# Optimization experiments

Hardware: AMD Instinct MI355X
Metric: run time of the kernel (lower is better)

Reference implementation:

```python
import math
import jax, jax.numpy as jnp
import numpy as np

B, N, D, H, L = 8, 1024, 512, 8, 6
HD = D // H
FREQ = 256
K_LORENTZ = 1.0


def lorentz_projx(x, k=K_LORENTZ):
    # geoopt Lorentz.projx: x0 = sqrt(k + ||x_space||^2)
    space = x[..., 1:]
    x0 = jnp.sqrt(k + jnp.sum(space * space, axis=-1, keepdims=True))
    return jnp.concatenate([x0, space], axis=-1)


def layernorm(x, eps=1e-6):
    m = jnp.mean(x, axis=-1, keepdims=True)
    v = jnp.mean((x - m) ** 2, axis=-1, keepdims=True)
    return (x - m) / jnp.sqrt(v + eps)


def make_pe(n, d):
    pos = np.arange(n, dtype=np.float32)[:, None]
    div = np.exp(np.arange(0, d, 2, dtype=np.float32) * (-math.log(10000.0) / d))
    pe = np.zeros((n, d), dtype=np.float32)
    pe[:, 0::2] = np.sin(pos * div)
    pe[:, 1::2] = np.cos(pos * div)
    return jnp.asarray(pe)


def setup_inputs() -> dict:
    key = jax.random.key(0)
    ks = jax.random.split(key, 20)
    s = 0.02
    inp = {
        "t": jax.random.uniform(ks[0], (B,), jnp.float32) * 1000.0,
        "x": jax.random.normal(ks[1], (B, N, D), jnp.float32),
        "mask": jnp.ones((B, N), jnp.float32),
        "pe": make_pe(N, D),
        # timestep embedder MLP (weights stored [in,out])
        "tw1": jax.random.normal(ks[2], (FREQ, D), jnp.float32) * s,
        "tb1": jnp.zeros((D,), jnp.float32),
        "tw2": jax.random.normal(ks[3], (D, D), jnp.float32) * s,
        "tb2": jnp.zeros((D,), jnp.float32),
        # per-layer params stacked over L
        "Wq": jax.random.normal(ks[4], (L, D, D), jnp.float32) * s,
        "bq": jnp.zeros((L, D), jnp.float32),
        "Wk": jax.random.normal(ks[5], (L, D, D), jnp.float32) * s,
        "bk": jnp.zeros((L, D), jnp.float32),
        "Wv": jax.random.normal(ks[6], (L, D, D), jnp.float32) * s,
        "bv": jnp.zeros((L, D), jnp.float32),
        "W1": jax.random.normal(ks[7], (L, D, 4 * D), jnp.float32) * s,
        "b1": jnp.zeros((L, 4 * D), jnp.float32),
        "W2": jax.random.normal(ks[8], (L, 4 * D, D), jnp.float32) * s,
        "b2": jnp.zeros((L, D), jnp.float32),
        "Wada": jax.random.normal(ks[9], (L, D, 6 * D), jnp.float32) * s,
        "bada": jnp.zeros((L, 6 * D), jnp.float32),
    }
    return inp


def timestep_embedding(t, dim=FREQ, max_period=10000.0):
    half = dim // 2
    freqs = jnp.exp(-math.log(max_period) * jnp.arange(half, dtype=jnp.float32) / half)
    args = t[:, None] * freqs[None]
    return jnp.concatenate([jnp.cos(args), jnp.sin(args)], axis=-1)  # [B, dim]


def attention(h, mask, Wq, bq, Wk, bk, Wv, bv):
    # h: [B,N,D], mask: [B,N]
    q = (h @ Wq + bq).reshape(B, N, H, HD).transpose(0, 2, 1, 3)
    k = (h @ Wk + bk).reshape(B, N, H, HD).transpose(0, 2, 1, 3)
    v = (h @ Wv + bv).reshape(B, N, H, HD).transpose(0, 2, 1, 3)
    scores = jnp.einsum("bhqd,bhkd->bhqk", q, k) / math.sqrt(HD)
    # faithful quirk: valid positions get +1 added, invalid get -10000
    mm = jnp.einsum("bi,bj->bij", mask, mask)[:, None]  # [B,1,N,N]
    mm = jnp.where(mm == 0, -10000.0, mm)
    scores = scores + mm
    probs = jax.nn.softmax(scores, axis=-1)
    ctx = jnp.einsum("bhqk,bhkd->bhqd", probs, v)
    return ctx.transpose(0, 2, 1, 3).reshape(B, N, D)


def reference(t, x, mask, pe, tw1, tb1, tw2, tb2, Wq, bq, Wk, bk, Wv, bv,
              W1, b1, W2, b2, Wada, bada):
    # z = x + PositionalEncoding(x) = 2*x + pe
    z = x + (x + pe[None])
    # timestep embedder
    c = timestep_embedding(t) @ tw1 + tb1
    c = jax.nn.silu(c) @ tw2 + tb2  # [B, D]
    for i in range(L):
        ada = jax.nn.silu(c) @ Wada[i] + bada[i]  # [B, 6D]
        sh_msa, sc_msa, g_msa, sh_mlp, sc_mlp, g_mlp = jnp.split(ada, 6, axis=-1)
        h = layernorm(z) * (1.0 + sc_msa[:, None]) + sh_msa[:, None]
        z = z + g_msa[:, None] * attention(h, mask, Wq[i], bq[i], Wk[i], bk[i], Wv[i], bv[i])
        z = lorentz_projx(z)
        h = layernorm(z) * (1.0 + sc_mlp[:, None]) + sh_mlp[:, None]
        m = jax.nn.gelu(h @ W1[i] + b1[i], approximate=True) @ W2[i] + b2[i]
        z = z + g_mlp[:, None] * m
        z = lorentz_projx(z)
    z = lorentz_projx(z)
    return jnp.where(mask[:, :, None] != 0, z, 0.0)
```

## Files before the change

kernel.cpp:

```cpp
#include <hip/hip_runtime.h>
#include <hip/hip_bf16.h>
#include <math.h>

#define NTOK 1024
#define DMODEL 512
#define NHEAD 8
#define HDIM 64
#define BATCH 8
#define NLAYER 6
#define ROWS (BATCH*NTOK)
#define QKVSTR 1536
#define LOG2E 1.44269504f

typedef __attribute__((ext_vector_type(8))) short bf16x8;
typedef __attribute__((ext_vector_type(4))) float f32x4;
typedef unsigned short ushort_t;


__device__ __forceinline__ float silu_f(float x) { return x / (1.f + expf(-x)); }

__device__ __forceinline__ float gelu_tanh_f(float x) {
    float x3 = x * x * x;
    float y2 = 1.5957691216057308f * (x + 0.044715f * x3);
    float e = __builtin_amdgcn_exp2f(-y2 * LOG2E);
    return x / (1.f + e);
}

__device__ __forceinline__ unsigned short f2bf(float x) {
    __hip_bfloat16 b = __float2bfloat16(x);
    return *reinterpret_cast<unsigned short*>(&b);
}

__device__ __forceinline__ float bf2f(unsigned short u) {
    union { float f; unsigned v; } c;
    c.v = (unsigned)u << 16;
    return c.f;
}

__device__ __forceinline__ float wave_sum(float v) {
    #pragma unroll
    for (int o = 1; o < 64; o <<= 1) v += __shfl_xor(v, o);
    return v;
}


__global__ __launch_bounds__(256) void init_z_kernel(const float* __restrict__ x,
                                                     const float* __restrict__ pe,
                                                     float* __restrict__ z) {
    int i = blockIdx.x * 256 + threadIdx.x;
    const int C4 = DMODEL / 4;
    int row = i / C4;
    int col4 = i - row * C4;
    int n = row & (NTOK - 1);
    float4 xv = ((const float4*)x)[i];
    float4 pv = ((const float4*)pe)[n * C4 + col4];
    float4 o;
    o.x = 2.f * xv.x + pv.x;
    o.y = 2.f * xv.y + pv.y;
    o.z = 2.f * xv.z + pv.z;
    o.w = 2.f * xv.w + pv.w;
    ((float4*)z)[i] = o;
}

__global__ void temb_kernel(const float* __restrict__ t, float* __restrict__ temb) {
    int b = blockIdx.x;
    int j = threadIdx.x;
    float f = expf(-9.210340371976184f * (float)j / 128.f);
    float a = t[b] * f;
    temb[b * 256 + j] = cosf(a);
    temb[b * 256 + 128 + j] = sinf(a);
}

__global__ void zero512(float* __restrict__ p) {
    p[blockIdx.x * 256 + threadIdx.x] = 0.f;
}

__global__ __launch_bounds__(256) void skinny_part(const float* __restrict__ A,
                                                   const float* __restrict__ W,
                                                   float* __restrict__ part,
                                                   int K, int N, int NL) {
    __shared__ float Als[8][128];
    const int l = blockIdx.z;
    const int n = blockIdx.x * 256 + threadIdx.x;
    const int kc = blockIdx.y;
    const int kbase = kc * 128;
    for (int i = threadIdx.x; i < 8 * 128; i += 256) {
        int b = i >> 7, k = i & 127;
        Als[b][k] = A[b * K + kbase + k];
    }
    __syncthreads();
    float acc[8] = {};
    const float* wp = W + (size_t)l * K * N + (size_t)kbase * N + n;
    for (int k = 0; k < 128; k += 4) {
        float w0 = wp[0];
        float w1 = wp[N];
        float w2 = wp[2 * N];
        float w3 = wp[3 * N];
        wp += 4 * (size_t)N;
        #pragma unroll
        for (int b = 0; b < 8; b++)
            acc[b] += Als[b][k] * w0 + Als[b][k + 1] * w1 + Als[b][k + 2] * w2 + Als[b][k + 3] * w3;
    }
    #pragma unroll
    for (int b = 0; b < 8; b++)
        part[((size_t)kc * 8 + b) * NL + (size_t)l * N + n] = acc[b];
}

template<int ACT>
__global__ __launch_bounds__(256) void skinny_reduce(const float* __restrict__ part,
                                                     const float* __restrict__ bias,
                                                     float* __restrict__ out,
                                                     int KC, int N, int NL) {
    int i = blockIdx.x * 256 + threadIdx.x;
    if (i >= 8 * NL) return;
    int b = i / NL, n = i - b * NL;
    float s = bias[n];
    for (int kc = 0; kc < KC; kc++) s += part[((size_t)kc * 8 + b) * NL + n];
    if (ACT == 1) s = silu_f(s);
    int l = n / N, nl = n - l * N;
    out[((size_t)l * 8 + b) * N + nl] = s;
}

__global__ __launch_bounds__(256) void transp_all(const float* __restrict__ Wq,
                                                  const float* __restrict__ Wk,
                                                  const float* __restrict__ Wv,
                                                  const float* __restrict__ W1,
                                                  const float* __restrict__ W2,
                                                  ushort_t* __restrict__ wqkv_t,
                                                  ushort_t* __restrict__ w1_t,
                                                  ushort_t* __restrict__ w2_t) {
    __shared__ float tile[32][33];
    const int L = blockIdx.z;
    Wq += (size_t)L * 512 * 512;
    Wk += (size_t)L * 512 * 512;
    Wv += (size_t)L * 512 * 512;
    W1 += (size_t)L * 512 * 2048;
    W2 += (size_t)L * 2048 * 512;
    wqkv_t += (size_t)L * QKVSTR * 512;
    w1_t += (size_t)L * 2048 * 512;
    w2_t += (size_t)L * 512 * 2048;
    int blk = blockIdx.x;
    const float* src; ushort_t* dst; int K, N, k0, n0;
    if (blk < 768) {
        int zz = blk >> 8, rem = blk & 255;
        k0 = (rem >> 4) * 32; n0 = (rem & 15) * 32;
        src = zz == 0 ? Wq : (zz == 1 ? Wk : Wv);
        dst = wqkv_t + zz * 512 * 512;
        K = 512; N = 512;
    } else if (blk < 1792) {
        int rem = blk - 768;
        n0 = (rem & 63) * 32; k0 = (rem >> 6) * 32;
        src = W1; dst = w1_t; K = 512; N = 2048;
    } else {
        int rem = blk - 1792;
        n0 = (rem & 15) * 32; k0 = (rem >> 4) * 32;
        src = W2; dst = w2_t; K = 2048; N = 512;
    }
    int c = threadIdx.x & 31, r8 = threadIdx.x >> 5;
    #pragma unroll
    for (int i = 0; i < 4; i++) {
        int r = r8 + i * 8;
        tile[r][c] = src[(size_t)(k0 + r) * N + n0 + c];
    }
    __syncthreads();
    #pragma unroll
    for (int i = 0; i < 4; i++) {
        int rr = r8 + i * 8;
        dst[(size_t)(n0 + rr) * K + k0 + c] = f2bf(tile[c][rr]);
    }
}

__global__ void pack_bias(const float* __restrict__ bq, const float* __restrict__ bk,
                          const float* __restrict__ bv, float* __restrict__ bqkv) {
    int idx = blockIdx.x * 256 + threadIdx.x;
    if (idx >= NLAYER * QKVSTR) return;
    int l = idx / QKVSTR, n = idx - l * QKVSTR;
    float v = (n < 512) ? bq[l * 512 + n] : (n < 1024) ? bk[l * 512 + n - 512] : bv[l * 512 + n - 1024];
    bqkv[idx] = v;
}

template<int ACT, int OUTBF, int QPRESCALE, int SPLITK>
__global__ __launch_bounds__(256) void mfma_gemm(const ushort_t* __restrict__ A,
                                                 const ushort_t* __restrict__ Bt,
                                                 const float* __restrict__ bias,
                                                 void* __restrict__ Cout,
                                                 int M, int N, int K) {
    __shared__ ushort_t smem[4 * 128 * 64];
    const int tid = threadIdx.x;
    const int lane = tid & 63, wv = tid >> 6;
    const int wm = (wv >> 1) * 64, wn = (wv & 1) * 64;
    const int lrow = lane & 15, lk = lane >> 4;
    const int m0 = blockIdx.x * 128, n0 = blockIdx.y * 128;
    const int srow = lane >> 3;
    const int qp = lane & 7;
    const int ql = qp ^ srow;

    int Keff = K;
    if (SPLITK) {
        Keff = K >> 1;
        const size_t koff = (size_t)blockIdx.z * Keff;
        A += koff;
        Bt += koff;
        Cout = (void*)((ushort_t*)Cout + (size_t)blockIdx.z * M * N);
    }

    f32x4 acc[4][4];
    #pragma unroll
    for (int i = 0; i < 4; i++)
        #pragma unroll
        for (int j = 0; j < 4; j++) {
            f32x4 zz = {0.f, 0.f, 0.f, 0.f};
            acc[i][j] = zz;
        }

    const int nK = Keff >> 6;

    auto STAGE = [&](int p, int ks) {
        const int k0 = ks << 6;
        ushort_t* Ad = smem + p * 8192;
        ushort_t* Bd = smem + 16384 + p * 8192;
        #pragma unroll
        for (int it = 0; it < 4; it++) {
            int chunk = wv * 4 + it;
            int row = chunk * 8 + srow;
            const ushort_t* srcA = A + (size_t)(m0 + row) * K + k0 + ql * 8;
            const ushort_t* srcB = Bt + (size_t)(n0 + row) * K + k0 + ql * 8;
            __builtin_amdgcn_global_load_lds((const __attribute__((address_space(1))) void*)srcA,
                                             (__attribute__((address_space(3))) void*)(Ad + chunk * 512),
                                             16, 0, 0);
            __builtin_amdgcn_global_load_lds((const __attribute__((address_space(1))) void*)srcB,
                                             (__attribute__((address_space(3))) void*)(Bd + chunk * 512),
                                             16, 0, 0);
        }
    };

    STAGE(0, 0);
    int cur = 0;
    for (int ks = 0; ks < nK; ks++) {
        if (ks + 1 < nK) {
            STAGE(cur ^ 1, ks + 1);
            asm volatile("s_waitcnt vmcnt(8)" ::: "memory");
        } else {
            asm volatile("s_waitcnt vmcnt(0)" ::: "memory");
        }
        __builtin_amdgcn_s_barrier();
        asm volatile("" ::: "memory");

        const ushort_t* Ab = smem + cur * 8192;
        const ushort_t* Bb = smem + 16384 + cur * 8192;
        #pragma unroll
        for (int kk = 0; kk < 2; kk++) {
            bf16x8 af[4], bfr[4];
            #pragma unroll
            for (int f = 0; f < 4; f++) {
                int ar = wm + f * 16 + lrow;
                af[f] = *(const bf16x8*)(Ab + ar * 64 + (((kk * 4 + lk) ^ (ar & 7)) << 3));
                int br = wn + f * 16 + lrow;
                bfr[f] = *(const bf16x8*)(Bb + br * 64 + (((kk * 4 + lk) ^ (br & 7)) << 3));
            }
            #pragma unroll
            for (int i = 0; i < 4; i++)
                #pragma unroll
                for (int j = 0; j < 4; j++)
                    acc[i][j] = __builtin_amdgcn_mfma_f32_16x16x32_bf16(af[i], bfr[j], acc[i][j], 0, 0, 0);
        }
        asm volatile("" ::: "memory");
        __builtin_amdgcn_s_barrier();
        cur ^= 1;
    }

    if (OUTBF) {
        __syncthreads();
        #pragma unroll
        for (int j = 0; j < 4; j++) {
            int coll = wn + j * 16 + lrow;
            float bcol = bias[n0 + coll];
            #pragma unroll
            for (int i = 0; i < 4; i++) {
                #pragma unroll
                for (int r = 0; r < 4; r++) {
                    int rowl = wm + i * 16 + lk * 4 + r;
                    float v = acc[i][j][r] + bcol;
                    if (ACT == 1) v = gelu_tanh_f(v);
                    if (QPRESCALE && (n0 + coll) < 512) v *= 0.125f * LOG2E;
                    smem[rowl * 136 + coll] = f2bf(v);
                }
            }
        }
        __syncthreads();
        ushort_t* Co = (ushort_t*)Cout;
        #pragma unroll
        for (int pass = 0; pass < 8; pass++) {
            int rowl = pass * 16 + (tid >> 4);
            int cseg = (tid & 15) * 8;
            uint4 vv = *(const uint4*)(smem + rowl * 136 + cseg);
            *(uint4*)(Co + (size_t)(m0 + rowl) * N + n0 + cseg) = vv;
        }
    } else {
        #pragma unroll
        for (int j = 0; j < 4; j++) {
            int col = n0 + wn + j * 16 + lrow;
            float bcol = bias[col];
            #pragma unroll
            for (int i = 0; i < 4; i++)
                #pragma unroll
                for (int r = 0; r < 4; r++) {
                    int row = m0 + wm + i * 16 + lk * 4 + r;
                    float v = acc[i][j][r] + bcol;
                    if (ACT == 1) v = gelu_tanh_f(v);
                    ((float*)Cout)[(size_t)row * N + col] = v;
                }
        }
    }
}


__global__ __launch_bounds__(256) void ln_mod_kernel(const float* __restrict__ z,
                                                     const float* __restrict__ ada,
                                                     ushort_t* __restrict__ out,
                                                     int sh_off, int sc_off) {
    int lane = threadIdx.x & 63;
    int row = blockIdx.x * 4 + (threadIdx.x >> 6);
    int b = row >> 10;
    const float4* zr = (const float4*)(z + (size_t)row * DMODEL);
    float4 va = zr[lane * 2], vb = zr[lane * 2 + 1];
    float s = va.x + va.y + va.z + va.w + vb.x + vb.y + vb.z + vb.w;
    float mean = wave_sum(s) * (1.f / DMODEL);
    float d0 = va.x - mean, d1 = va.y - mean, d2 = va.z - mean, d3 = va.w - mean;
    float d4 = vb.x - mean, d5 = vb.y - mean, d6 = vb.z - mean, d7 = vb.w - mean;
    float ssq = d0*d0 + d1*d1 + d2*d2 + d3*d3 + d4*d4 + d5*d5 + d6*d6 + d7*d7;
    float rstd = rsqrtf(wave_sum(ssq) * (1.f / DMODEL) + 1e-6f);
    const float* ab = ada + b * (6 * DMODEL);
    const float4* scp = (const float4*)(ab + sc_off);
    const float4* shp = (const float4*)(ab + sh_off);
    float4 sca = scp[lane * 2], scb = scp[lane * 2 + 1];
    float4 sha = shp[lane * 2], shb = shp[lane * 2 + 1];
    uint4 pk;
    pk.x = (unsigned)f2bf(d0 * rstd * (1.f + sca.x) + sha.x) |
           ((unsigned)f2bf(d1 * rstd * (1.f + sca.y) + sha.y) << 16);
    pk.y = (unsigned)f2bf(d2 * rstd * (1.f + sca.z) + sha.z) |
           ((unsigned)f2bf(d3 * rstd * (1.f + sca.w) + sha.w) << 16);
    pk.z = (unsigned)f2bf(d4 * rstd * (1.f + scb.x) + shb.x) |
           ((unsigned)f2bf(d5 * rstd * (1.f + scb.y) + shb.y) << 16);
    pk.w = (unsigned)f2bf(d6 * rstd * (1.f + scb.z) + shb.z) |
           ((unsigned)f2bf(d7 * rstd * (1.f + scb.w) + shb.w) << 16);
    ((uint4*)(out + (size_t)row * DMODEL))[lane] = pk;
}

template<int TWO>
__global__ __launch_bounds__(256) void resid_ln_kernel(float* __restrict__ z,
                                                       const ushort_t* __restrict__ add,
                                                       const ushort_t* __restrict__ add2,
                                                       const float* __restrict__ abias,
                                                       const float* __restrict__ adaG, int g_off,
                                                       const float* __restrict__ adaLN, int sh_off, int sc_off,
                                                       ushort_t* __restrict__ out) {
    int lane = threadIdx.x & 63;
    int row = blockIdx.x * 4 + (threadIdx.x >> 6);
    int b = row >> 10;
    float4* zr = (float4*)(z + (size_t)row * DMODEL);
    float4 va = zr[lane * 2], vb = zr[lane * 2 + 1];
    uint4 a4 = ((const uint4*)(add + (size_t)row * DMODEL))[lane];
    const float4* gp = (const float4*)(adaG + b * (6 * DMODEL) + g_off);
    float4 ga = gp[lane * 2], gb = gp[lane * 2 + 1];
    const ushort_t* e = (const ushort_t*)&a4;
    float av[8];
    #pragma unroll
    for (int i = 0; i < 8; i++) av[i] = bf2f(e[i]);
    if (TWO) {
        uint4 a42 = ((const uint4*)(add2 + (size_t)row * DMODEL))[lane];
        const ushort_t* e2 = (const ushort_t*)&a42;
        float4 ba = ((const float4*)abias)[lane * 2];
        float4 bb = ((const float4*)abias)[lane * 2 + 1];
        av[0] += bf2f(e2[0]) + ba.x; av[1] += bf2f(e2[1]) + ba.y;
        av[2] += bf2f(e2[2]) + ba.z; av[3] += bf2f(e2[3]) + ba.w;
        av[4] += bf2f(e2[4]) + bb.x; av[5] += bf2f(e2[5]) + bb.y;
        av[6] += bf2f(e2[6]) + bb.z; av[7] += bf2f(e2[7]) + bb.w;
    }
    va.x += ga.x * av[0]; va.y += ga.y * av[1];
    va.z += ga.z * av[2]; va.w += ga.w * av[3];
    vb.x += gb.x * av[4]; vb.y += gb.y * av[5];
    vb.z += gb.z * av[6]; vb.w += gb.w * av[7];
    float ssq = va.x*va.x + va.y*va.y + va.z*va.z + va.w*va.w
              + vb.x*vb.x + vb.y*vb.y + vb.z*vb.z + vb.w*vb.w;
    if (lane == 0) ssq -= va.x * va.x;
    float tot = wave_sum(ssq);
    if (lane == 0) va.x = sqrtf(1.f + tot);
    zr[lane * 2] = va; zr[lane * 2 + 1] = vb;
    float s = va.x + va.y + va.z + va.w + vb.x + vb.y + vb.z + vb.w;
    float mean = wave_sum(s) * (1.f / DMODEL);
    float d0 = va.x - mean, d1 = va.y - mean, d2 = va.z - mean, d3 = va.w - mean;
    float d4 = vb.x - mean, d5 = vb.y - mean, d6 = vb.z - mean, d7 = vb.w - mean;
    float sq2 = d0*d0 + d1*d1 + d2*d2 + d3*d3 + d4*d4 + d5*d5 + d6*d6 + d7*d7;
    float rstd = rsqrtf(wave_sum(sq2) * (1.f / DMODEL) + 1e-6f);
    const float* ab = adaLN + b * (6 * DMODEL);
    const float4* scp = (const float4*)(ab + sc_off);
    const float4* shp = (const float4*)(ab + sh_off);
    float4 sca = scp[lane * 2], scb = scp[lane * 2 + 1];
    float4 sha = shp[lane * 2], shb = shp[lane * 2 + 1];
    uint4 pk;
    pk.x = (unsigned)f2bf(d0 * rstd * (1.f + sca.x) + sha.x) |
           ((unsigned)f2bf(d1 * rstd * (1.f + sca.y) + sha.y) << 16);
    pk.y = (unsigned)f2bf(d2 * rstd * (1.f + sca.z) + sha.z) |
           ((unsigned)f2bf(d3 * rstd * (1.f + sca.w) + sha.w) << 16);
    pk.z = (unsigned)f2bf(d4 * rstd * (1.f + scb.x) + shb.x) |
           ((unsigned)f2bf(d5 * rstd * (1.f + scb.y) + shb.y) << 16);
    pk.w = (unsigned)f2bf(d6 * rstd * (1.f + scb.z) + shb.z) |
           ((unsigned)f2bf(d7 * rstd * (1.f + scb.w) + shb.w) << 16);
    ((uint4*)(out + (size_t)row * DMODEL))[lane] = pk;
}

__global__ __launch_bounds__(256) void resid_final_kernel(const float* __restrict__ z,
                                                          const ushort_t* __restrict__ add,
                                                          const ushort_t* __restrict__ add2,
                                                          const float* __restrict__ abias,
                                                          const float* __restrict__ adaG, int g_off,
                                                          const float* __restrict__ mask,
                                                          float* __restrict__ out) {
    int lane = threadIdx.x & 63;
    int row = blockIdx.x * 4 + (threadIdx.x >> 6);
    int b = row >> 10;
    const float4* zr = (const float4*)(z + (size_t)row * DMODEL);
    float4 va = zr[lane * 2], vb = zr[lane * 2 + 1];
    uint4 a4 = ((const uint4*)(add + (size_t)row * DMODEL))[lane];
    uint4 a42 = ((const uint4*)(add2 + (size_t)row * DMODEL))[lane];
    const float4* gp = (const float4*)(adaG + b * (6 * DMODEL) + g_off);
    float4 ga = gp[lane * 2], gb = gp[lane * 2 + 1];
    const ushort_t* e = (const ushort_t*)&a4;
    const ushort_t* e2 = (const ushort_t*)&a42;
    float4 ba = ((const float4*)abias)[lane * 2];
    float4 bb = ((const float4*)abias)[lane * 2 + 1];
    va.x += ga.x * (bf2f(e[0]) + bf2f(e2[0]) + ba.x);
    va.y += ga.y * (bf2f(e[1]) + bf2f(e2[1]) + ba.y);
    va.z += ga.z * (bf2f(e[2]) + bf2f(e2[2]) + ba.z);
    va.w += ga.w * (bf2f(e[3]) + bf2f(e2[3]) + ba.w);
    vb.x += gb.x * (bf2f(e[4]) + bf2f(e2[4]) + bb.x);
    vb.y += gb.y * (bf2f(e[5]) + bf2f(e2[5]) + bb.y);
    vb.z += gb.z * (bf2f(e[6]) + bf2f(e2[6]) + bb.z);
    vb.w += gb.w * (bf2f(e[7]) + bf2f(e2[7]) + bb.w);
    float ssq = va.x*va.x + va.y*va.y + va.z*va.z + va.w*va.w
              + vb.x*vb.x + vb.y*vb.y + vb.z*vb.z + vb.w*vb.w;
    if (lane == 0) ssq -= va.x * va.x;
    float tot = wave_sum(ssq);
    if (lane == 0) va.x = sqrtf(1.f + tot);
    float m = mask[row];
    if (m == 0.f) {
        va.x = va.y = va.z = va.w = 0.f;
        vb.x = vb.y = vb.z = vb.w = 0.f;
    }
    float4* orow = (float4*)(out + (size_t)row * DMODEL);
    orow[lane * 2] = va; orow[lane * 2 + 1] = vb;
}

__global__ __launch_bounds__(512) void flash_attn_mfma(const ushort_t* __restrict__ qkv,
                                                       const float* __restrict__ mask,
                                                       ushort_t* __restrict__ ctx) {
    __shared__ ushort_t Kls[64 * 64];
    __shared__ ushort_t Vt[64 * 64];
    __shared__ ushort_t Pls[8][16 * 64];
    __shared__ float Mall[NTOK];

    const int tid = threadIdx.x;
    const int lane = tid & 63, w = tid >> 6;
    const int c = lane & 15, g = lane >> 4;
    const int bh = blockIdx.x;
    const int q0 = blockIdx.y * 128;
    const int b = bh >> 3, h = bh & 7;

    const ushort_t* qptr = qkv + (size_t)(b * NTOK + q0 + w * 16 + c) * QKVSTR + h * HDIM + g * 8;
    bf16x8 aq0 = *(const bf16x8*)(qptr);
    bf16x8 aq1 = *(const bf16x8*)(qptr + 32);

    const float mq = mask[b * NTOK + q0 + w * 16 + c];

    #pragma unroll
    for (int i = 0; i < 2; i++) Mall[tid + i * 512] = mask[b * NTOK + tid + i * 512];

    f32x4 o[4];
    #pragma unroll
    for (int j = 0; j < 4; j++) { f32x4 zz = {0.f,0.f,0.f,0.f}; o[j] = zz; }
    float l_run = 0.f;

    const int srow = lane >> 3, qp = lane & 7, ql = qp ^ srow;
    const int kp = tid & 31, dg = tid >> 5;

    char* Pw = (char*)&Pls[w][0];
    const int cswz = (c & 7) << 4;

    for (int kt = 0; kt < NTOK / 64; kt++) {
        const int k0 = kt * 64;
        __syncthreads();
        {
            int row = w * 8 + srow;
            const ushort_t* src = qkv + (size_t)(b * NTOK + k0 + row) * QKVSTR + 512 + h * HDIM + ql * 8;
            __builtin_amdgcn_global_load_lds((const __attribute__((address_space(1))) void*)src,
                                             (__attribute__((address_space(3))) void*)(Kls + w * 512),
                                             16, 0, 0);
        }
        {
            const ushort_t* v0 = qkv + (size_t)(b * NTOK + k0 + 2 * kp) * QKVSTR + 1024 + h * HDIM + dg * 4;
            uint2 r0 = *(const uint2*)v0;
            uint2 r1 = *(const uint2*)(v0 + QKVSTR);
            const ushort_t* e0 = (const ushort_t*)&r0;
            const ushort_t* e1 = (const ushort_t*)&r1;
            unsigned* VtU = (unsigned*)Vt;
            #pragma unroll
            for (int i = 0; i < 4; i++) {
                int d = dg * 4 + i;
                unsigned pk = (unsigned)e0[i] | ((unsigned)e1[i] << 16);
                VtU[d * 32 + (((kp >> 2) ^ (d & 7)) << 2) + (kp & 3)] = pk;
            }
        }
        __syncthreads();

        f32x4 s[4];
        #pragma unroll
        for (int j = 0; j < 4; j++) { f32x4 zz = {0.f,0.f,0.f,0.f}; s[j] = zz; }
        __builtin_amdgcn_s_setprio(1);
        #pragma unroll
        for (int j = 0; j < 4; j++) {
            int row = j * 16 + c;
            bf16x8 ak0 = *(const bf16x8*)(Kls + row * 64 + ((g ^ (row & 7)) << 3));
            bf16x8 ak1 = *(const bf16x8*)(Kls + row * 64 + (((4 + g) ^ (row & 7)) << 3));
            s[j] = __builtin_amdgcn_mfma_f32_16x16x32_bf16(ak0, aq0, s[j], 0, 0, 0);
            s[j] = __builtin_amdgcn_mfma_f32_16x16x32_bf16(ak1, aq1, s[j], 0, 0, 0);
        }
        __builtin_amdgcn_s_setprio(0);

        #pragma unroll
        for (int j = 0; j < 4; j++) {
            float4 mk4 = *(const float4*)&Mall[k0 + j * 16 + 4 * g];
            const float* mkp = (const float*)&mk4;
            float p[4];
            #pragma unroll
            for (int r = 0; r < 4; r++) {
                float mm = mq * mkp[r];
                float sv = s[j][r] + (mm == 0.f ? -14427.0f : mm * LOG2E);
                p[r] = exp2f(sv);
                l_run += p[r];
            }
            uint2 pk2;
            pk2.x = (unsigned)f2bf(p[0]) | ((unsigned)f2bf(p[1]) << 16);
            pk2.y = (unsigned)f2bf(p[2]) | ((unsigned)f2bf(p[3]) << 16);
            *(uint2*)(Pw + c * 128 + ((j * 32 + g * 8) ^ cswz)) = pk2;
        }

        __builtin_amdgcn_s_setprio(1);
        #pragma unroll
        for (int kk = 0; kk < 2; kk++) {
            bf16x8 pa = *(const bf16x8*)(Pw + c * 128 + ((kk * 64 + g * 16) ^ cswz));
            #pragma unroll
            for (int j = 0; j < 4; j++) {
                int vr = j * 16 + c;
                bf16x8 bv = *(const bf16x8*)(Vt + vr * 64 + (((kk * 4 + g) ^ (vr & 7)) << 3));
                o[j] = __builtin_amdgcn_mfma_f32_16x16x32_bf16(pa, bv, o[j], 0, 0, 0);
            }
        }
        __builtin_amdgcn_s_setprio(0);
    }

    l_run += __shfl_xor(l_run, 16);
    l_run += __shfl_xor(l_run, 32);

    float invr[4];
    #pragma unroll
    for (int r = 0; r < 4; r++) invr[r] = 1.f / __shfl(l_run, (g << 4) + 4 * g + r);
    #pragma unroll
    for (int r = 0; r < 4; r++) {
        size_t row = (size_t)(b * NTOK + q0 + w * 16 + 4 * g + r) * DMODEL + h * HDIM;
        #pragma unroll
        for (int j = 0; j < 4; j++)
            ctx[row + j * 16 + c] = f2bf(o[j][r] * invr[r]);
    }
}


extern "C" void kernel_launch(void* const* d_in, const int* in_sizes, int n_in,
                              void* d_out, int out_size, void* d_ws, size_t ws_size,
                              hipStream_t stream) {
    const float* t    = (const float*)d_in[0];
    const float* x    = (const float*)d_in[1];
    const float* mask = (const float*)d_in[2];
    const float* pe   = (const float*)d_in[3];
    const float* tw1  = (const float*)d_in[4];
    const float* tb1  = (const float*)d_in[5];
    const float* tw2  = (const float*)d_in[6];
    const float* tb2  = (const float*)d_in[7];
    const float* Wq   = (const float*)d_in[8];
    const float* bq   = (const float*)d_in[9];
    const float* Wk   = (const float*)d_in[10];
    const float* bk   = (const float*)d_in[11];
    const float* Wv   = (const float*)d_in[12];
    const float* bv   = (const float*)d_in[13];
    const float* W1   = (const float*)d_in[14];
    const float* b1   = (const float*)d_in[15];
    const float* W2   = (const float*)d_in[16];
    const float* b2   = (const float*)d_in[17];
    const float* Wada = (const float*)d_in[18];
    const float* bada = (const float*)d_in[19];
    float* out = (float*)d_out;

    const bool hoist = ws_size >= 113129472ull;
    const int WL = hoist ? NLAYER : 1;

    float* z      = (float*)d_ws;
    ushort_t* cxb = (ushort_t*)(z + (size_t)ROWS * DMODEL);
    ushort_t* cxb2 = cxb + (size_t)ROWS * DMODEL;
    ushort_t* qkv = cxb2 + (size_t)ROWS * DMODEL;
    ushort_t* mid = qkv;
    ushort_t* hb  = qkv + (size_t)ROWS * 2048;
    ushort_t* wqkv_t = hb + (size_t)ROWS * DMODEL;
    ushort_t* w1_t   = wqkv_t + (size_t)WL * QKVSTR * 512;
    ushort_t* w2_t   = w1_t + (size_t)WL * 2048 * 512;
    float* bqkv  = (float*)(w2_t + (size_t)WL * 512 * 2048);
    float* fzero = bqkv + NLAYER * QKVSTR;
    float* temb  = fzero + 512;
    float* cmid  = temb + BATCH * 256;
    float* scs   = cmid + BATCH * DMODEL;
    float* part  = scs + BATCH * DMODEL;
    float* ada_all = part + 4 * 8 * (NLAYER * 3072);

    init_z_kernel<<<ROWS * DMODEL / 4 / 256, 256, 0, stream>>>(x, pe, z);
    temb_kernel<<<BATCH, 128, 0, stream>>>(t, temb);
    pack_bias<<<(NLAYER * QKVSTR + 255) / 256, 256, 0, stream>>>(bq, bk, bv, bqkv);
    zero512<<<2, 256, 0, stream>>>(fzero);

    skinny_part<<<dim3(2, 2, 1), 256, 0, stream>>>(temb, tw1, part, 256, 512, 512);
    skinny_reduce<1><<<16, 256, 0, stream>>>(part, tb1, cmid, 2, 512, 512);
    skinny_part<<<dim3(2, 4, 1), 256, 0, stream>>>(cmid, tw2, part, 512, 512, 512);
    skinny_reduce<1><<<16, 256, 0, stream>>>(part, tb2, scs, 4, 512, 512);
    skinny_part<<<dim3(12, 4, NLAYER), 256, 0, stream>>>(scs, Wada, part, 512, 3072, NLAYER * 3072);
    skinny_reduce<0><<<(8 * NLAYER * 3072 + 255) / 256, 256, 0, stream>>>(
        part, bada, ada_all, 4, 3072, NLAYER * 3072);

    if (hoist) {
        transp_all<<<dim3(2816, 1, NLAYER), 256, 0, stream>>>(Wq, Wk, Wv, W1, W2,
                                                              wqkv_t, w1_t, w2_t);
    }

    dim3 gqkv(ROWS / 128, QKVSTR / 128);
    dim3 gmlp1(ROWS / 128, 2048 / 128);
    dim3 gmlp2(ROWS / 128, DMODEL / 128, 2);
    dim3 ga(BATCH * NHEAD, NTOK / 128);

    ln_mod_kernel<<<ROWS / 4, 256, 0, stream>>>(z, ada_all, hb, 0, 512);

    for (int i = 0; i < NLAYER; i++) {
        const float* ada = ada_all + (size_t)i * 8 * 3072;

        const ushort_t* wq_i = hoist ? wqkv_t + (size_t)i * QKVSTR * 512 : wqkv_t;
        const ushort_t* w1_i = hoist ? w1_t + (size_t)i * 2048 * 512 : w1_t;
        const ushort_t* w2_i = hoist ? w2_t + (size_t)i * 512 * 2048 : w2_t;

        if (!hoist) {
            transp_all<<<dim3(2816, 1, 1), 256, 0, stream>>>(Wq + (size_t)i * 512 * 512,
                                                             Wk + (size_t)i * 512 * 512,
                                                             Wv + (size_t)i * 512 * 512,
                                                             W1 + (size_t)i * 512 * 2048,
                                                             W2 + (size_t)i * 2048 * 512,
                                                             wqkv_t, w1_t, w2_t);
        }

        mfma_gemm<0, 1, 1, 0><<<gqkv, 256, 0, stream>>>(hb, wq_i, bqkv + i * QKVSTR, qkv,
                                                        ROWS, QKVSTR, DMODEL);

        flash_attn_mfma<<<ga, 512, 0, stream>>>(qkv, mask, cxb);

        resid_ln_kernel<0><<<ROWS / 4, 256, 0, stream>>>(z, cxb, nullptr, nullptr,
                                                         ada, 2 * DMODEL,
                                                         ada, 3 * DMODEL, 4 * DMODEL, hb);

        mfma_gemm<1, 1, 0, 0><<<gmlp1, 256, 0, stream>>>(hb, w1_i, b1 + (size_t)i * 4 * DMODEL, mid,
                                                         ROWS, 4 * DMODEL, DMODEL);
        mfma_gemm<0, 1, 0, 1><<<gmlp2, 256, 0, stream>>>(mid, w2_i, fzero, cxb,
                                                         ROWS, DMODEL, 4 * DMODEL);

        if (i < NLAYER - 1) {
            const float* adan = ada_all + (size_t)(i + 1) * 8 * 3072;
            resid_ln_kernel<1><<<ROWS / 4, 256, 0, stream>>>(z, cxb, cxb2, b2 + (size_t)i * DMODEL,
                                                             ada, 5 * DMODEL,
                                                             adan, 0, 512, hb);
        } else {
            resid_final_kernel<<<ROWS / 4, 256, 0, stream>>>(z, cxb, cxb2, b2 + (size_t)i * DMODEL,
                                                             ada, 5 * DMODEL, mask, out);
        }
    }
}
```

Measured before the change: 911.8 us.

## Write V pre-transposed from QKV GEMM epilogue and async-load it in attention

The QKV GEMM epilogue now writes Q and K into a packed 1024-wide buffer and stores V transposed per head as [b,h,d,token]. The flash attention kernel can then fetch V tiles with global_load_lds, using the same XOR swizzle as K, instead of doing scalar loads plus an in-register transpose into LDS. This removes per-tile transpose work and uncoalesced V loads from the attention inner loop. The cost moves to the GEMM epilogue, which now does strided column reads from LDS for V blocks and may hit bank conflicts there.

```diff
diff --git a/kernel.cpp b/kernel.cpp
--- a/kernel.cpp
+++ b/kernel.cpp
@@ -10,6 +10,7 @@
 #define NLAYER 6
 #define ROWS (BATCH*NTOK)
 #define QKVSTR 1536
+#define QKSTR 1024
 #define LOG2E 1.44269504f
 
 typedef __attribute__((ext_vector_type(8))) short bf16x8;
@@ -179,12 +180,13 @@
     bqkv[idx] = v;
 }
 
-template<int ACT, int OUTBF, int QPRESCALE, int SPLITK>
+template<int ACT, int OUTBF, int QPRESCALE, int SPLITK, int VSPLIT>
 __global__ __launch_bounds__(256) void mfma_gemm(const ushort_t* __restrict__ A,
                                                  const ushort_t* __restrict__ Bt,
                                                  const float* __restrict__ bias,
                                                  void* __restrict__ Cout,
-                                                 int M, int N, int K) {
+                                                 ushort_t* __restrict__ vtout,
+                                                 int M, int N, int K, int CS) {
     __shared__ ushort_t smem[4 * 128 * 64];
     const int tid = threadIdx.x;
     const int lane = tid & 63, wv = tid >> 6;
@@ -201,7 +203,7 @@
         const size_t koff = (size_t)blockIdx.z * Keff;
         A += koff;
         Bt += koff;
-        Cout = (void*)((ushort_t*)Cout + (size_t)blockIdx.z * M * N);
+        Cout = (void*)((ushort_t*)Cout + (size_t)blockIdx.z * M * CS);
     }
 
     f32x4 acc[4][4];
@@ -288,13 +290,30 @@
             }
         }
         __syncthreads();
-        ushort_t* Co = (ushort_t*)Cout;
-        #pragma unroll
-        for (int pass = 0; pass < 8; pass++) {
-            int rowl = pass * 16 + (tid >> 4);
-            int cseg = (tid & 15) * 8;
-            uint4 vv = *(const uint4*)(smem + rowl * 136 + cseg);
-            *(uint4*)(Co + (size_t)(m0 + rowl) * N + n0 + cseg) = vv;
+        if (VSPLIT && n0 >= 1024) {
+            int col_l = tid & 127, seg = tid >> 7;
+            int local = n0 + col_l - 1024;
+            int hh = local >> 6, d = local & 63;
+            int bb = m0 >> 10;
+            int tokb = (m0 & 1023) + seg * 64;
+            ushort_t* dst = vtout + (((size_t)(bb * 8 + hh) * 64 + d) << 10) + tokb;
+            #pragma unroll
+            for (int ch = 0; ch < 8; ch++) {
+                ushort_t tmp[8];
+                #pragma unroll
+                for (int r = 0; r < 8; r++)
+                    tmp[r] = smem[(seg * 64 + ch * 8 + r) * 136 + col_l];
+                *(uint4*)(dst + ch * 8) = *(const uint4*)tmp;
+            }
+        } else {
+            ushort_t* Co = (ushort_t*)Cout;
+            #pragma unroll
+            for (int pass = 0; pass < 8; pass++) {
+                int rowl = pass * 16 + (tid >> 4);
+                int cseg = (tid & 15) * 8;
+                uint4 vv = *(const uint4*)(smem + rowl * 136 + cseg);
+                *(uint4*)(Co + (size_t)(m0 + rowl) * CS + n0 + cseg) = vv;
+            }
         }
     } else {
         #pragma unroll
@@ -308,7 +327,7 @@
                     int row = m0 + wm + i * 16 + lk * 4 + r;
                     float v = acc[i][j][r] + bcol;
                     if (ACT == 1) v = gelu_tanh_f(v);
-                    ((float*)Cout)[(size_t)row * N + col] = v;
+                    ((float*)Cout)[(size_t)row * CS + col] = v;
                 }
         }
     }
@@ -452,7 +471,8 @@
     orow[lane * 2] = va; orow[lane * 2 + 1] = vb;
 }
 
-__global__ __launch_bounds__(512) void flash_attn_mfma(const ushort_t* __restrict__ qkv,
+__global__ __launch_bounds__(512) void flash_attn_mfma(const ushort_t* __restrict__ qk,
+                                                       const ushort_t* __restrict__ vT,
                                                        const float* __restrict__ mask,
                                                        ushort_t* __restrict__ ctx) {
     __shared__ ushort_t Kls[64 * 64];
@@ -467,7 +487,7 @@
     const int q0 = blockIdx.y * 128;
     const int b = bh >> 3, h = bh & 7;
 
-    const ushort_t* qptr = qkv + (size_t)(b * NTOK + q0 + w * 16 + c) * QKVSTR + h * HDIM + g * 8;
+    const ushort_t* qptr = qk + (size_t)(b * NTOK + q0 + w * 16 + c) * QKSTR + h * HDIM + g * 8;
     bf16x8 aq0 = *(const bf16x8*)(qptr);
     bf16x8 aq1 = *(const bf16x8*)(qptr + 32);
 
@@ -482,7 +502,7 @@
     float l_run = 0.f;
 
     const int srow = lane >> 3, qp = lane & 7, ql = qp ^ srow;
-    const int kp = tid & 31, dg = tid >> 5;
+    const ushort_t* vbase = vT + ((size_t)(bh * 64 + w * 8 + srow) << 10) + ql * 8;
 
     char* Pw = (char*)&Pls[w][0];
     const int cswz = (c & 7) << 4;
@@ -492,24 +512,16 @@
         __syncthreads();
         {
             int row = w * 8 + srow;
-            const ushort_t* src = qkv + (size_t)(b * NTOK + k0 + row) * QKVSTR + 512 + h * HDIM + ql * 8;
+            const ushort_t* src = qk + (size_t)(b * NTOK + k0 + row) * QKSTR + 512 + h * HDIM + ql * 8;
             __builtin_amdgcn_global_load_lds((const __attribute__((address_space(1))) void*)src,
                                              (__attribute__((address_space(3))) void*)(Kls + w * 512),
                                              16, 0, 0);
         }
         {
-            const ushort_t* v0 = qkv + (size_t)(b * NTOK + k0 + 2 * kp) * QKVSTR + 1024 + h * HDIM + dg * 4;
-            uint2 r0 = *(const uint2*)v0;
-            uint2 r1 = *(const uint2*)(v0 + QKVSTR);
-            const ushort_t* e0 = (const ushort_t*)&r0;
-            const ushort_t* e1 = (const ushort_t*)&r1;
-            unsigned* VtU = (unsigned*)Vt;
-            #pragma unroll
-            for (int i = 0; i < 4; i++) {
-                int d = dg * 4 + i;
-                unsigned pk = (unsigned)e0[i] | ((unsigned)e1[i] << 16);
-                VtU[d * 32 + (((kp >> 2) ^ (d & 7)) << 2) + (kp & 3)] = pk;
-            }
+            const ushort_t* src = vbase + k0;
+            __builtin_amdgcn_global_load_lds((const __attribute__((address_space(1))) void*)src,
+                                             (__attribute__((address_space(3))) void*)(Vt + w * 512),
+                                             16, 0, 0);
         }
         __syncthreads();
 
@@ -606,9 +618,10 @@
     float* z      = (float*)d_ws;
     ushort_t* cxb = (ushort_t*)(z + (size_t)ROWS * DMODEL);
     ushort_t* cxb2 = cxb + (size_t)ROWS * DMODEL;
-    ushort_t* qkv = cxb2 + (size_t)ROWS * DMODEL;
-    ushort_t* mid = qkv;
-    ushort_t* hb  = qkv + (size_t)ROWS * 2048;
+    ushort_t* mid = cxb2 + (size_t)ROWS * DMODEL;
+    ushort_t* qk  = mid;
+    ushort_t* vT  = mid + (size_t)ROWS * QKSTR;
+    ushort_t* hb  = mid + (size_t)ROWS * 2048;
     ushort_t* wqkv_t = hb + (size_t)ROWS * DMODEL;
     ushort_t* w1_t   = wqkv_t + (size_t)WL * QKVSTR * 512;
     ushort_t* w2_t   = w1_t + (size_t)WL * 2048 * 512;
@@ -661,19 +674,19 @@
                                                              wqkv_t, w1_t, w2_t);
         }
 
-        mfma_gemm<0, 1, 1, 0><<<gqkv, 256, 0, stream>>>(hb, wq_i, bqkv + i * QKVSTR, qkv,
-                                                        ROWS, QKVSTR, DMODEL);
-
-        flash_attn_mfma<<<ga, 512, 0, stream>>>(qkv, mask, cxb);
+        mfma_gemm<0, 1, 1, 0, 1><<<gqkv, 256, 0, stream>>>(hb, wq_i, bqkv + i * QKVSTR,
+                                                           qk, vT, ROWS, QKVSTR, DMODEL, QKSTR);
+
+        flash_attn_mfma<<<ga, 512, 0, stream>>>(qk, vT, mask, cxb);
 
         resid_ln_kernel<0><<<ROWS / 4, 256, 0, stream>>>(z, cxb, nullptr, nullptr,
                                                          ada, 2 * DMODEL,
                                                          ada, 3 * DMODEL, 4 * DMODEL, hb);
 
-        mfma_gemm<1, 1, 0, 0><<<gmlp1, 256, 0, stream>>>(hb, w1_i, b1 + (size_t)i * 4 * DMODEL, mid,
-                                                         ROWS, 4 * DMODEL, DMODEL);
-        mfma_gemm<0, 1, 0, 1><<<gmlp2, 256, 0, stream>>>(mid, w2_i, fzero, cxb,
-                                                         ROWS, DMODEL, 4 * DMODEL);
+        mfma_gemm<1, 1, 0, 0, 0><<<gmlp1, 256, 0, stream>>>(hb, w1_i, b1 + (size_t)i * 4 * DMODEL,
+                                                            mid, nullptr, ROWS, 4 * DMODEL, DMODEL, 2048);
+        mfma_gemm<0, 1, 0, 1, 0><<<gmlp2, 256, 0, stream>>>(mid, w2_i, fzero,
+                                                            cxb, nullptr, ROWS, DMODEL, 4 * DMODEL, DMODEL);
 
         if (i < NLAYER - 1) {
             const float* adan = ada_all + (size_t)(i + 1) * 8 * 3072;
```

After: 935.0 us. 2.6% more time.
